# Performance work log

Measured on AMD Instinct MI355X. Metric: run time of the kernel, lower is better.

The kernel has to match this reference:

```python
import jax, jax.numpy as jnp
import numpy as np

N = 50000
E = 600000
D = 128        # in_dim == hidden_dim
L = 3          # num_layers
BN_EPS = 1e-5


def setup_inputs() -> dict:
    key = jax.random.key(0)
    ks = jax.random.split(key, 12)
    x = jax.random.normal(ks[0], (N, D), dtype=jnp.float32)
    edge_index = jax.random.randint(ks[1], (2, E), 0, N, dtype=jnp.int64)
    s = 1.0 / np.sqrt(D)
    # SAGEConv per layer: out = lin_l(mean_aggr(x_src)) + lin_r(x_root); bias on lin_l only
    Wl = jax.random.uniform(ks[2], (L, D, D), jnp.float32, -s, s)
    Wr = jax.random.uniform(ks[3], (L, D, D), jnp.float32, -s, s)
    bl = jax.random.uniform(ks[4], (L, D), jnp.float32, -s, s)
    gamma = jnp.ones((L, D), jnp.float32)
    beta = jnp.zeros((L, D), jnp.float32)
    h = D // 2
    s2 = 1.0 / np.sqrt(h)
    W1 = jax.random.uniform(ks[5], (D, h), jnp.float32, -s, s)
    b1 = jax.random.uniform(ks[6], (h,), jnp.float32, -s, s)
    W2 = jax.random.uniform(ks[7], (h, 2), jnp.float32, -s2, s2)
    b2 = jax.random.uniform(ks[8], (2,), jnp.float32, -s2, s2)
    return {"x": x, "edge_index": edge_index, "Wl": Wl, "Wr": Wr, "bl": bl,
            "gamma": gamma, "beta": beta, "W1": W1, "b1": b1, "W2": W2, "b2": b2}


def _sage_layer(x, src, dst, Wl, Wr, bl):
    # mean aggregation of source features into destination nodes
    msg = x[src]                                            # [E, D] gather
    summed = jax.ops.segment_sum(msg, dst, num_segments=N)  # [N, D]
    cnt = jax.ops.segment_sum(jnp.ones((E,), x.dtype), dst, num_segments=N)
    mean = summed / jnp.maximum(cnt, 1.0)[:, None]
    return mean @ Wl + bl + x @ Wr


def _bn(x, gamma, beta):
    mu = jnp.mean(x, axis=0)
    var = jnp.mean(jnp.square(x - mu), axis=0)  # biased var (torch BN)
    return (x - mu) * (gamma / jnp.sqrt(var + BN_EPS)) + beta


def reference(x, edge_index, Wl, Wr, bl, gamma, beta, W1, b1, W2, b2):
    src, dst = edge_index[0], edge_index[1]
    h = x
    for i in range(L):
        h = _sage_layer(h, src, dst, Wl[i], Wr[i], bl[i])
        h = _bn(h, gamma[i], beta[i])
        h = jax.nn.relu(h)
        # dropout: identity at inference
    z = jax.nn.relu(h @ W1 + b1)
    logits = z @ W2 + b2
    return logits, jax.nn.softmax(logits, axis=-1)
```

## Files before the change

kernel.cpp:

```cpp
#include <hip/hip_runtime.h>
#include <math.h>

#define N_NODES 50000
#define N_EDGES 600000
#define D 128
#define NLAYERS 3
#define BN_EPS 1e-5f
#define NBLK ((N_NODES + 255) / 256)
#define GBLK ((N_NODES + 63) / 64)
#define NW (NLAYERS * 128 * 256)
#define MPAD 136

typedef short short8 __attribute__((ext_vector_type(8)));
typedef float f32x4 __attribute__((ext_vector_type(4)));

__device__ __forceinline__ float b2f(unsigned short u) {
    return __uint_as_float(((unsigned int)u) << 16);
}
__device__ __forceinline__ unsigned short f2b(float f) {
    unsigned int b = __float_as_uint(f);
    return (unsigned short)((b + 0x7fffu + ((b >> 16) & 1u)) >> 16);
}

__global__ void k_cvt_x(const float* __restrict__ x, unsigned short* __restrict__ xb) {
    int idx = blockIdx.x * 256 + threadIdx.x;
    if (idx >= N_NODES * D / 4) return;
    float4 v = ((const float4*)x)[idx];
    ushort4 o;
    o.x = f2b(v.x); o.y = f2b(v.y); o.z = f2b(v.z); o.w = f2b(v.w);
    ((ushort4*)xb)[idx] = o;
}

__global__ void k_cvt_weights(const float* __restrict__ Wl, const float* __restrict__ Wr,
                              const float* __restrict__ W1, unsigned short* __restrict__ Wt,
                              unsigned short* __restrict__ W1t) {
    int idx = blockIdx.x * 256 + threadIdx.x;
    if (idx < NW) {
        int l = idx >> 15;
        int rem = idx & 32767;
        int c = rem >> 8;
        int k = rem & 255;
        float v = (k < 128) ? Wl[l * 16384 + k * 128 + c]
                            : Wr[l * 16384 + (k - 128) * 128 + c];
        Wt[idx] = f2b(v);
    } else {
        int i = idx - NW;
        if (i < 64 * 128) {
            int c = i >> 7;
            int k = i & 127;
            W1t[i] = f2b(W1[k * 64 + c]);
        }
    }
}

__global__ void k_hist(const int* __restrict__ dst, int* __restrict__ cnt) {
    int e = blockIdx.x * blockDim.x + threadIdx.x;
    if (e < N_EDGES) atomicAdd(&cnt[dst[e]], 1);
}

__global__ void k_local_scan(const int* __restrict__ cnt, int* __restrict__ row_ptr,
                             int* __restrict__ bsum) {
    __shared__ int sm[256];
    int tid = threadIdx.x;
    int i = blockIdx.x * 256 + tid;
    int v = (i < N_NODES) ? cnt[i] : 0;
    sm[tid] = v;
    __syncthreads();
    for (int off = 1; off < 256; off <<= 1) {
        int t = (tid >= off) ? sm[tid - off] : 0;
        __syncthreads();
        sm[tid] += t;
        __syncthreads();
    }
    int incl = sm[tid];
    if (i < N_NODES) row_ptr[i] = incl - v;
    if (tid == 255) bsum[blockIdx.x] = incl;
}

__global__ void k_scan_bsums(const int* __restrict__ bsum, int* __restrict__ boff,
                             int* __restrict__ row_ptr) {
    __shared__ int sm[256];
    int tid = threadIdx.x;
    int v = (tid < NBLK) ? bsum[tid] : 0;
    sm[tid] = v;
    __syncthreads();
    for (int off = 1; off < 256; off <<= 1) {
        int t = (tid >= off) ? sm[tid - off] : 0;
        __syncthreads();
        sm[tid] += t;
        __syncthreads();
    }
    int incl = sm[tid];
    if (tid < NBLK) boff[tid] = incl - v;
    if (tid == 255) row_ptr[N_NODES] = incl;
}

__global__ void k_add_off(int* __restrict__ row_ptr, const int* __restrict__ boff,
                          int* __restrict__ row_fill) {
    int i = blockIdx.x * 256 + threadIdx.x;
    if (i < N_NODES) {
        int v = row_ptr[i] + boff[i >> 8];
        row_ptr[i] = v;
        row_fill[i] = v;
    }
}

__global__ void k_fill(const int* __restrict__ src, const int* __restrict__ dst,
                       int* __restrict__ row_fill, int* __restrict__ edge_sorted) {
    int e = blockIdx.x * blockDim.x + threadIdx.x;
    if (e < N_EDGES) {
        int pos = atomicAdd(&row_fill[dst[e]], 1);
        edge_sorted[pos] = src[e];
    }
}

__global__ __launch_bounds__(256) void k_layer(const unsigned short* __restrict__ h,
                                               const int* __restrict__ edge_sorted,
                                               const int* __restrict__ row_ptr,
                                               const unsigned short* __restrict__ Wt,
                                               const float* __restrict__ bias,
                                               float* __restrict__ pre,
                                               float* __restrict__ sums) {
    __shared__ unsigned short meanb[64][MPAD];
    __shared__ float red[4][256];

    int tid = threadIdx.x;
    int row0 = blockIdx.x * 64;

    {
        int sub = tid >> 4;
        int lane = tid & 15;
        const short8* hp = (const short8*)h;
#pragma unroll
        for (int p = 0; p < 4; ++p) {
            int nl = p * 16 + sub;
            int node = row0 + nl;
            if (node < N_NODES) {
                int beg = row_ptr[node], end = row_ptr[node + 1];
                float a[8];
#pragma unroll
                for (int i = 0; i < 8; ++i) a[i] = 0.f;
                int e1 = end - 1;
                for (int j = beg; j < end; j += 4) {
                    int j1 = j + 1, j2 = j + 2, j3 = j + 3;
                    int i1 = (j1 <= e1) ? j1 : e1;
                    int i2 = (j2 <= e1) ? j2 : e1;
                    int i3 = (j3 <= e1) ? j3 : e1;
                    int s0 = edge_sorted[j];
                    int s1 = edge_sorted[i1];
                    int s2 = edge_sorted[i2];
                    int s3 = edge_sorted[i3];
                    short8 v0 = hp[(size_t)s0 * 16 + lane];
                    short8 v1 = hp[(size_t)s1 * 16 + lane];
                    short8 v2 = hp[(size_t)s2 * 16 + lane];
                    short8 v3 = hp[(size_t)s3 * 16 + lane];
                    float m1 = (j1 < end) ? 1.f : 0.f;
                    float m2 = (j2 < end) ? 1.f : 0.f;
                    float m3 = (j3 < end) ? 1.f : 0.f;
#pragma unroll
                    for (int i = 0; i < 8; ++i) {
                        float t = a[i] + b2f((unsigned short)v0[i]);
                        t = fmaf(m1, b2f((unsigned short)v1[i]), t);
                        t = fmaf(m2, b2f((unsigned short)v2[i]), t);
                        t = fmaf(m3, b2f((unsigned short)v3[i]), t);
                        a[i] = t;
                    }
                }
                float inv = 1.0f / fmaxf((float)(end - beg), 1.0f);
                short8 o;
#pragma unroll
                for (int i = 0; i < 8; ++i) o[i] = (short)f2b(a[i] * inv);
                *(short8*)&meanb[nl][lane * 8] = o;
            }
        }
    }
    __syncthreads();

    int wave = tid >> 6;
    int lane = tid & 63;
    int col = lane & 15;
    int quad = lane >> 4;
    int row_base = row0 + wave * 16;
    bool valid = row_base < N_NODES;

    f32x4 acc[8];
#pragma unroll
    for (int t = 0; t < 8; ++t) acc[t] = (f32x4){0.f, 0.f, 0.f, 0.f};

    if (valid) {
        int arow_l = wave * 16 + col;
        int arow_g = row_base + col;
#pragma unroll
        for (int kk = 0; kk < 8; ++kk) {
            short8 a;
            if (kk < 4) {
                a = *(const short8*)&meanb[arow_l][kk * 32 + quad * 8];
            } else {
                a = *(const short8*)(h + (size_t)arow_g * D + (kk - 4) * 32 + quad * 8);
            }
#pragma unroll
            for (int t = 0; t < 8; ++t) {
                short8 b = *(const short8*)(Wt + (size_t)(t * 16 + col) * 256 + kk * 32 + quad * 8);
                acc[t] = __builtin_amdgcn_mfma_f32_16x16x32_bf16(a, b, acc[t], 0, 0, 0);
            }
        }
    }

#pragma unroll
    for (int t = 0; t < 8; ++t) {
        float s = 0.f, ss = 0.f;
        if (valid) {
            float bc = bias[t * 16 + col];
#pragma unroll
            for (int r = 0; r < 4; ++r) {
                float v = acc[t][r] + bc;
                pre[(size_t)(row_base + quad * 4 + r) * D + t * 16 + col] = v;
                s += v;
                ss += v * v;
            }
        }
        s += __shfl_xor(s, 16);  ss += __shfl_xor(ss, 16);
        s += __shfl_xor(s, 32);  ss += __shfl_xor(ss, 32);
        if (quad == 0) {
            red[wave][t * 16 + col] = s;
            red[wave][128 + t * 16 + col] = ss;
        }
    }
    __syncthreads();
    float pv = red[0][tid] + red[1][tid] + red[2][tid] + red[3][tid];
    atomicAdd(&sums[tid], pv);
}

__global__ void k_bnrelu(const float* __restrict__ pre, const float* __restrict__ sums,
                         const float* __restrict__ gamma, const float* __restrict__ beta,
                         unsigned short* __restrict__ outbuf) {
    int idx = blockIdx.x * blockDim.x + threadIdx.x;
    const int total = N_NODES * D / 4;
    if (idx >= total) return;
    const float* sumsq = sums + 128;
    int col4 = (idx & 31) * 4;
    float4 v = ((const float4*)pre)[idx];
    float vv[4] = {v.x, v.y, v.z, v.w};
    unsigned short o[4];
    const float invN = 1.0f / (float)N_NODES;
#pragma unroll
    for (int c = 0; c < 4; ++c) {
        int j = col4 + c;
        float mu  = sums[j] * invN;
        float var = sumsq[j] * invN - mu * mu;
        float sc = gamma[j] * rsqrtf(var + BN_EPS);
        float sh = beta[j] - mu * sc;
        float x = vv[c] * sc + sh;
        o[c] = f2b(fmaxf(x, 0.f));
    }
    ushort4 ov; ov.x = o[0]; ov.y = o[1]; ov.z = o[2]; ov.w = o[3];
    ((ushort4*)outbuf)[idx] = ov;
}

__global__ __launch_bounds__(256) void k_mlp_mfma(const unsigned short* __restrict__ h,
                                                  const unsigned short* __restrict__ W1t,
                                                  const float* __restrict__ b1,
                                                  const float* __restrict__ W2,
                                                  const float* __restrict__ b2,
                                                  float* __restrict__ out) {
    int wave = threadIdx.x >> 6;
    int lane = threadIdx.x & 63;
    int col = lane & 15;
    int quad = lane >> 4;
    int row_base = blockIdx.x * 64 + wave * 16;
    if (row_base >= N_NODES) return;
    int arow = row_base + col;

    f32x4 acc[4];
#pragma unroll
    for (int t = 0; t < 4; ++t) acc[t] = (f32x4){0.f, 0.f, 0.f, 0.f};

#pragma unroll
    for (int kk = 0; kk < 4; ++kk) {
        short8 a = *(const short8*)(h + (size_t)arow * D + kk * 32 + quad * 8);
#pragma unroll
        for (int t = 0; t < 4; ++t) {
            short8 b = *(const short8*)(W1t + (size_t)(t * 16 + col) * 128 + kk * 32 + quad * 8);
            acc[t] = __builtin_amdgcn_mfma_f32_16x16x32_bf16(a, b, acc[t], 0, 0, 0);
        }
    }

    float pa[4] = {0.f, 0.f, 0.f, 0.f}, pb[4] = {0.f, 0.f, 0.f, 0.f};
#pragma unroll
    for (int t = 0; t < 4; ++t) {
        int c = t * 16 + col;
        float bb = b1[c];
        float w2a = W2[c * 2], w2b = W2[c * 2 + 1];
#pragma unroll
        for (int r = 0; r < 4; ++r) {
            float z = fmaxf(acc[t][r] + bb, 0.f);
            pa[r] = fmaf(z, w2a, pa[r]);
            pb[r] = fmaf(z, w2b, pb[r]);
        }
    }
#pragma unroll
    for (int m = 1; m < 16; m <<= 1) {
#pragma unroll
        for (int r = 0; r < 4; ++r) {
            pa[r] += __shfl_xor(pa[r], m);
            pb[r] += __shfl_xor(pb[r], m);
        }
    }
    if (col < 4) {
        int node = row_base + quad * 4 + col;
        float l0 = pa[col] + b2[0], l1 = pb[col] + b2[1];
        float2 lg; lg.x = l0; lg.y = l1;
        ((float2*)out)[node] = lg;
        float m = fmaxf(l0, l1);
        float e0 = expf(l0 - m), e1 = expf(l1 - m);
        float s = 1.0f / (e0 + e1);
        float2 pr; pr.x = e0 * s; pr.y = e1 * s;
        ((float2*)(out + 2 * N_NODES))[node] = pr;
    }
}

extern "C" void kernel_launch(void* const* d_in, const int* in_sizes, int n_in,
                              void* d_out, int out_size, void* d_ws, size_t ws_size,
                              hipStream_t stream) {
    const float* x     = (const float*)d_in[0];
    const int*   ei    = (const int*)d_in[1];
    const int*   src   = ei;
    const int*   dst   = ei + N_EDGES;
    const float* Wl    = (const float*)d_in[2];
    const float* Wr    = (const float*)d_in[3];
    const float* bl    = (const float*)d_in[4];
    const float* gamma = (const float*)d_in[5];
    const float* beta  = (const float*)d_in[6];
    const float* W1    = (const float*)d_in[7];
    const float* b1    = (const float*)d_in[8];
    const float* W2    = (const float*)d_in[9];
    const float* b2    = (const float*)d_in[10];
    float* out = (float*)d_out;

    char* ws = (char*)d_ws;
    size_t off = 0;
    auto alloc = [&](size_t bytes) -> void* {
        void* p = ws + off;
        off += (bytes + 255) & ~(size_t)255;
        return p;
    };
    unsigned short* xb   = (unsigned short*)alloc((size_t)N_NODES * D * 2);
    unsigned short* Ha   = (unsigned short*)alloc((size_t)N_NODES * D * 2);
    float* pre           = (float*)alloc((size_t)N_NODES * D * 4);
    unsigned short* Wtb  = (unsigned short*)alloc((size_t)NW * 2);
    unsigned short* W1t  = (unsigned short*)alloc((size_t)64 * 128 * 2);
    int* cnt             = (int*)alloc((size_t)N_NODES * 4);
    int* row_ptr         = (int*)alloc((size_t)(N_NODES + 1) * 4);
    int* row_fill        = (int*)alloc((size_t)N_NODES * 4);
    int* edge_sorted     = (int*)alloc((size_t)N_EDGES * 4);
    int* bsum            = (int*)alloc((size_t)NBLK * 4);
    int* boff            = (int*)alloc((size_t)NBLK * 4);
    float* sums_all      = (float*)alloc(NLAYERS * 256 * 4);

    k_cvt_x<<<(N_NODES * D / 4 + 255) / 256, 256, 0, stream>>>(x, xb);
    k_cvt_weights<<<(NW + 64 * 128 + 255) / 256, 256, 0, stream>>>(Wl, Wr, W1, Wtb, W1t);

    hipMemsetAsync(cnt, 0, (size_t)N_NODES * 4, stream);
    k_hist<<<(N_EDGES + 255) / 256, 256, 0, stream>>>(dst, cnt);
    k_local_scan<<<NBLK, 256, 0, stream>>>(cnt, row_ptr, bsum);
    k_scan_bsums<<<1, 256, 0, stream>>>(bsum, boff, row_ptr);
    k_add_off<<<NBLK, 256, 0, stream>>>(row_ptr, boff, row_fill);
    k_fill<<<(N_EDGES + 255) / 256, 256, 0, stream>>>(src, dst, row_fill, edge_sorted);

    hipMemsetAsync(sums_all, 0, NLAYERS * 256 * 4, stream);

    const unsigned short* hcur = xb;
    unsigned short* hout[3] = {Ha, xb, Ha};
    for (int l = 0; l < NLAYERS; ++l) {
        float* sums = sums_all + l * 256;
        k_layer<<<GBLK, 256, 0, stream>>>(hcur, edge_sorted, row_ptr,
                                          Wtb + (size_t)l * 32768, bl + l * D, pre, sums);
        k_bnrelu<<<(N_NODES * D / 4 + 255) / 256, 256, 0, stream>>>(
            pre, sums, gamma + l * D, beta + l * D, hout[l]);
        hcur = hout[l];
    }

    k_mlp_mfma<<<GBLK, 256, 0, stream>>>(hcur, W1t, b1, W2, b2, out);
}
```

Measured before the change: 387.7 us.

## Split fused aggregate+GEMM layer into wave-per-node aggregation and separate MFMA GEMM

Splits the fused layer kernel into two kernels. The first aggregates neighbours with one wave per node: four edge slots of 16 lanes each gather in parallel, and the partial sums are reduced with cross-lane shuffles. The mean is written to a new global bf16 buffer, which a separate MFMA GEMM kernel then reads. This is meant to expose more memory-level parallelism in the gather and balance the per-node work across waves. The cost is an extra round trip of the N×D mean buffer through global memory and one extra kernel launch per layer.

```diff
diff --git a/kernel.cpp b/kernel.cpp
--- a/kernel.cpp
+++ b/kernel.cpp
@@ -9,7 +9,6 @@
 #define NBLK ((N_NODES + 255) / 256)
 #define GBLK ((N_NODES + 63) / 64)
 #define NW (NLAYERS * 128 * 256)
-#define MPAD 136
 
 typedef short short8 __attribute__((ext_vector_type(8)));
 typedef float f32x4 __attribute__((ext_vector_type(4)));
@@ -114,73 +113,66 @@
     }
 }
 
-__global__ __launch_bounds__(256) void k_layer(const unsigned short* __restrict__ h,
-                                               const int* __restrict__ edge_sorted,
-                                               const int* __restrict__ row_ptr,
-                                               const unsigned short* __restrict__ Wt,
-                                               const float* __restrict__ bias,
-                                               float* __restrict__ pre,
-                                               float* __restrict__ sums) {
-    __shared__ unsigned short meanb[64][MPAD];
+__global__ __launch_bounds__(256) void k_agg(const unsigned short* __restrict__ h,
+                                             const int* __restrict__ edge_sorted,
+                                             const int* __restrict__ row_ptr,
+                                             unsigned short* __restrict__ meanbuf) {
+    int node = blockIdx.x * 4 + (threadIdx.x >> 6);
+    if (node >= N_NODES) return;
+    int lane  = threadIdx.x & 63;
+    int eslot = lane >> 4;
+    int c16   = lane & 15;
+    int beg = row_ptr[node], end = row_ptr[node + 1];
+    int deg = end - beg;
+    const short8* hp = (const short8*)h;
+    float a[8];
+#pragma unroll
+    for (int i = 0; i < 8; ++i) a[i] = 0.f;
+    int e1 = end - 1;
+    for (int base = beg; base < end; base += 8) {
+        int j0 = base + eslot;
+        int j1 = j0 + 4;
+        int i0 = (j0 <= e1) ? j0 : e1;
+        int i1 = (j1 <= e1) ? j1 : e1;
+        int s0 = edge_sorted[i0];
+        int s1 = edge_sorted[i1];
+        short8 v0 = hp[(size_t)s0 * 16 + c16];
+        short8 v1 = hp[(size_t)s1 * 16 + c16];
+        float m0 = (j0 < end) ? 1.f : 0.f;
+        float m1 = (j1 < end) ? 1.f : 0.f;
+#pragma unroll
+        for (int i = 0; i < 8; ++i) {
+            float t = fmaf(m0, b2f((unsigned short)v0[i]), a[i]);
+            a[i] = fmaf(m1, b2f((unsigned short)v1[i]), t);
+        }
+    }
+#pragma unroll
+    for (int i = 0; i < 8; ++i) {
+        a[i] += __shfl_xor(a[i], 16);
+        a[i] += __shfl_xor(a[i], 32);
+    }
+    if (eslot == 0) {
+        float inv = 1.0f / fmaxf((float)deg, 1.0f);
+        short8 o;
+#pragma unroll
+        for (int i = 0; i < 8; ++i) o[i] = (short)f2b(a[i] * inv);
+        ((short8*)meanbuf)[(size_t)node * 16 + c16] = o;
+    }
+}
+
+__global__ __launch_bounds__(256) void k_gemm_mfma(const unsigned short* __restrict__ Am,
+                                                   const unsigned short* __restrict__ Ah,
+                                                   const unsigned short* __restrict__ Wt,
+                                                   const float* __restrict__ bias,
+                                                   float* __restrict__ pre,
+                                                   float* __restrict__ sums) {
     __shared__ float red[4][256];
-
     int tid = threadIdx.x;
-    int row0 = blockIdx.x * 64;
-
-    {
-        int sub = tid >> 4;
-        int lane = tid & 15;
-        const short8* hp = (const short8*)h;
-#pragma unroll
-        for (int p = 0; p < 4; ++p) {
-            int nl = p * 16 + sub;
-            int node = row0 + nl;
-            if (node < N_NODES) {
-                int beg = row_ptr[node], end = row_ptr[node + 1];
-                float a[8];
-#pragma unroll
-                for (int i = 0; i < 8; ++i) a[i] = 0.f;
-                int e1 = end - 1;
-                for (int j = beg; j < end; j += 4) {
-                    int j1 = j + 1, j2 = j + 2, j3 = j + 3;
-                    int i1 = (j1 <= e1) ? j1 : e1;
-                    int i2 = (j2 <= e1) ? j2 : e1;
-                    int i3 = (j3 <= e1) ? j3 : e1;
-                    int s0 = edge_sorted[j];
-                    int s1 = edge_sorted[i1];
-                    int s2 = edge_sorted[i2];
-                    int s3 = edge_sorted[i3];
-                    short8 v0 = hp[(size_t)s0 * 16 + lane];
-                    short8 v1 = hp[(size_t)s1 * 16 + lane];
-                    short8 v2 = hp[(size_t)s2 * 16 + lane];
-                    short8 v3 = hp[(size_t)s3 * 16 + lane];
-                    float m1 = (j1 < end) ? 1.f : 0.f;
-                    float m2 = (j2 < end) ? 1.f : 0.f;
-                    float m3 = (j3 < end) ? 1.f : 0.f;
-#pragma unroll
-                    for (int i = 0; i < 8; ++i) {
-                        float t = a[i] + b2f((unsigned short)v0[i]);
-                        t = fmaf(m1, b2f((unsigned short)v1[i]), t);
-                        t = fmaf(m2, b2f((unsigned short)v2[i]), t);
-                        t = fmaf(m3, b2f((unsigned short)v3[i]), t);
-                        a[i] = t;
-                    }
-                }
-                float inv = 1.0f / fmaxf((float)(end - beg), 1.0f);
-                short8 o;
-#pragma unroll
-                for (int i = 0; i < 8; ++i) o[i] = (short)f2b(a[i] * inv);
-                *(short8*)&meanb[nl][lane * 8] = o;
-            }
-        }
-    }
-    __syncthreads();
-
     int wave = tid >> 6;
     int lane = tid & 63;
     int col = lane & 15;
     int quad = lane >> 4;
-    int row_base = row0 + wave * 16;
+    int row_base = blockIdx.x * 64 + wave * 16;
     bool valid = row_base < N_NODES;
 
     f32x4 acc[8];
@@ -188,16 +180,12 @@
     for (int t = 0; t < 8; ++t) acc[t] = (f32x4){0.f, 0.f, 0.f, 0.f};
 
     if (valid) {
-        int arow_l = wave * 16 + col;
-        int arow_g = row_base + col;
+        int arow = row_base + col;
 #pragma unroll
         for (int kk = 0; kk < 8; ++kk) {
-            short8 a;
-            if (kk < 4) {
-                a = *(const short8*)&meanb[arow_l][kk * 32 + quad * 8];
-            } else {
-                a = *(const short8*)(h + (size_t)arow_g * D + (kk - 4) * 32 + quad * 8);
-            }
+            const unsigned short* Aptr = (kk < 4) ? Am : Ah;
+            int kofs = (kk & 3) * 32 + quad * 8;
+            short8 a = *(const short8*)(Aptr + (size_t)arow * D + kofs);
 #pragma unroll
             for (int t = 0; t < 8; ++t) {
                 short8 b = *(const short8*)(Wt + (size_t)(t * 16 + col) * 256 + kk * 32 + quad * 8);
@@ -346,6 +334,7 @@
     };
     unsigned short* xb   = (unsigned short*)alloc((size_t)N_NODES * D * 2);
     unsigned short* Ha   = (unsigned short*)alloc((size_t)N_NODES * D * 2);
+    unsigned short* Mb   = (unsigned short*)alloc((size_t)N_NODES * D * 2);
     float* pre           = (float*)alloc((size_t)N_NODES * D * 4);
     unsigned short* Wtb  = (unsigned short*)alloc((size_t)NW * 2);
     unsigned short* W1t  = (unsigned short*)alloc((size_t)64 * 128 * 2);
@@ -373,8 +362,9 @@
     unsigned short* hout[3] = {Ha, xb, Ha};
     for (int l = 0; l < NLAYERS; ++l) {
         float* sums = sums_all + l * 256;
-        k_layer<<<GBLK, 256, 0, stream>>>(hcur, edge_sorted, row_ptr,
-                                          Wtb + (size_t)l * 32768, bl + l * D, pre, sums);
+        k_agg<<<(N_NODES + 3) / 4, 256, 0, stream>>>(hcur, edge_sorted, row_ptr, Mb);
+        k_gemm_mfma<<<GBLK, 256, 0, stream>>>(Mb, hcur, Wtb + (size_t)l * 32768,
+                                              bl + l * D, pre, sums);
         k_bnrelu<<<(N_NODES * D / 4 + 255) / 256, 256, 0, stream>>>(
             pre, sums, gamma + l * D, beta + l * D, hout[l]);
         hcur = hout[l];
```

Measured after the change: 410.6 us. 5.9% more time.
